# Performance work log

Measured on AMD Instinct MI355X. Metric: run time of the kernel, lower is better.

Reference implementation:

```python
import jax, jax.numpy as jnp
import numpy as np
import math

D_EMB = 1024
N_HEADS = 16
SCALE = 0.02
B, T = 4, 2048


def _norm(x):
    # torch.std_mean default: unbiased std (ddof=1) over last dim
    m = jnp.mean(x, axis=-1, keepdims=True)
    s = jnp.std(x, axis=-1, keepdims=True, ddof=1)
    return (x - m) / (s + 1e-05)


def setup_inputs() -> dict:
    key = jax.random.key(0)
    kx, kw = jax.random.split(key)
    x = jax.random.normal(kx, (B, D_EMB, T), dtype=jnp.float32)
    qkv = jax.random.normal(kw, (3, N_HEADS, D_EMB, D_EMB // N_HEADS), dtype=jnp.float32) * SCALE
    return {"x": x, "qkv": qkv}


def reference(x, qkv):
    Bsz, D, Tlen = x.shape
    H = qkv.shape[1]
    # (3, B, H, T, d_head)
    h = jnp.einsum('bdt,nhde->nbhte', x, qkv)
    q, k, v = h[0], h[1], h[2]
    q = _norm(q)
    k = _norm(k)
    scale = math.sqrt(D // H)  # torch: sqrt(d_emb // H)
    attn = jnp.einsum('bhte,bhse->bhts', q, k) / scale  # [B,H,T,T]
    attn = jax.nn.softmax(attn, axis=-1)
    out = jnp.einsum('bhts,bhse->bhet', attn, v)  # [B,H,d_head,T]
    return out.reshape(Bsz, D, Tlen)
```

## Files before the change

### kernel.cpp

```cpp
#include <hip/hip_runtime.h>
#include <hip/hip_bf16.h>

#define B_SZ 4
#define NHEADS 16
#define T_SZ 2048
#define DE 1024
#define DH 64
#define BH (B_SZ*NHEADS)
#define SCL 0.18033688011112042f

typedef __attribute__((ext_vector_type(8))) short short8;
typedef __attribute__((ext_vector_type(4))) float float4v;
typedef __attribute__((ext_vector_type(2))) unsigned int uint2v;

__device__ __forceinline__ short f2bf(float f) {
    __hip_bfloat16 h = __float2bfloat16(f);
    return *reinterpret_cast<short*>(&h);
}
__device__ __forceinline__ unsigned int pack_bf2(float a, float b) {
    float2 f; f.x = a; f.y = b;
    __hip_bfloat162 h = __float22bfloat162_rn(f);
    return *reinterpret_cast<unsigned int*>(&h);
}
__device__ __forceinline__ float4v zero4() {
    float4v z = {0.f, 0.f, 0.f, 0.f};
    return z;
}
__device__ __forceinline__ int swz(int row, int g) {
    return row * 64 + (((g) ^ (row & 7)) << 3);
}
__device__ __forceinline__ void gl_lds16(const short* g, short* l) {
    __builtin_amdgcn_global_load_lds(
        (const __attribute__((address_space(1))) void*)g,
        (__attribute__((address_space(3))) void*)l, 16, 0, 0);
}

__global__ __launch_bounds__(256) void transpose_k(const float* __restrict__ src,
                                                   short* __restrict__ dst,
                                                   int R, int C) {
    __shared__ __align__(16) short tile[64 * 65];
    int c0 = blockIdx.x * 64, r0 = blockIdx.y * 64;
    src += (size_t)blockIdx.z * R * C;
    dst += (size_t)blockIdx.z * R * C;
    int tid = threadIdx.x;
#pragma unroll
    for (int it = 0; it < 16; ++it) {
        int idx = it * 256 + tid;
        int rr = idx >> 6, cc = idx & 63;
        tile[cc * 65 + rr] = f2bf(src[(size_t)(r0 + rr) * C + c0 + cc]);
    }
    __syncthreads();
#pragma unroll
    for (int it = 0; it < 16; ++it) {
        int idx = it * 256 + tid;
        int cc = idx >> 6, rr = idx & 63;
        dst[(size_t)(c0 + cc) * R + r0 + rr] = tile[cc * 65 + rr];
    }
}

__global__ __launch_bounds__(256, 2) void qkv_k(const short* __restrict__ XT,
                                                const short* __restrict__ WT,
                                                short* __restrict__ Qw,
                                                short* __restrict__ Kw,
                                                short* __restrict__ Vt) {
    __shared__ __align__(16) short ldsA[2][128 * 64];
    __shared__ __align__(16) short ldsB[2][128 * 64];
    int b  = blockIdx.x >> 4;
    int t0 = (blockIdx.x & 15) * 128;
    int n  = blockIdx.y >> 3;
    int h0 = (blockIdx.y & 7) * 2;
    int tid = threadIdx.x, wave = tid >> 6, lane = tid & 63;
    int l15 = lane & 15, quad = lane >> 4;
    int wr = wave >> 1, wc = wave & 1;

    const short* Arow = XT + ((size_t)b * T_SZ + t0) * DE;
    const short* Brow = WT + ((size_t)n * 1024 + h0 * 64) * DE;

    int rA = lane >> 3;
    int gl = (lane & 7) ^ rA;

    float4v acc[4][4];
#pragma unroll
    for (int mm = 0; mm < 4; ++mm)
#pragma unroll
        for (int j = 0; j < 4; ++j) acc[mm][j] = zero4();

    auto STAGE = [&](short* La, short* Lb, int k0) {
#pragma unroll
        for (int it = 0; it < 4; ++it) {
            int rowbase = it * 32 + wave * 8;
            gl_lds16(&Arow[(size_t)(rowbase + rA) * DE + k0 + gl * 8],
                     &La[(it * 256 + wave * 64) * 8]);
            gl_lds16(&Brow[(size_t)(rowbase + rA) * DE + k0 + gl * 8],
                     &Lb[(it * 256 + wave * 64) * 8]);
        }
    };
    auto COMPUTE = [&](const short* La, const short* Lb) {
#pragma unroll
        for (int ks = 0; ks < 2; ++ks) {
            short8 af[4], bf[4];
#pragma unroll
            for (int mm = 0; mm < 4; ++mm)
                af[mm] = *(const short8*)&La[swz(64 * wr + 16 * mm + l15, 4 * ks + quad)];
#pragma unroll
            for (int j = 0; j < 4; ++j)
                bf[j] = *(const short8*)&Lb[swz(64 * wc + 16 * j + l15, 4 * ks + quad)];
#pragma unroll
            for (int mm = 0; mm < 4; ++mm)
#pragma unroll
                for (int j = 0; j < 4; ++j)
                    acc[mm][j] = __builtin_amdgcn_mfma_f32_16x16x32_bf16(af[mm], bf[j], acc[mm][j], 0, 0, 0);
        }
    };

    STAGE(ldsA[0], ldsB[0], 0);
    __syncthreads();
    for (int k0 = 0; k0 < DE; k0 += 128) {
        STAGE(ldsA[1], ldsB[1], k0 + 64);
        COMPUTE(ldsA[0], ldsB[0]);
        __syncthreads();
        if (k0 + 128 < DE)
            STAGE(ldsA[0], ldsB[0], k0 + 128);
        COMPUTE(ldsA[1], ldsB[1]);
        __syncthreads();
    }

    int h = h0 + wc;
    int bh = b * NHEADS + h;
#pragma unroll
    for (int mm = 0; mm < 4; ++mm) {
        int tbase = t0 + 64 * wr + 16 * mm;
        if (n < 2) {
            float oscale = (n == 0) ? SCL : 1.0f;
            float mu[4], inv[4];
#pragma unroll
            for (int r = 0; r < 4; ++r) {
                float s1 = 0.f, s2 = 0.f;
#pragma unroll
                for (int jj = 0; jj < 4; ++jj) {
                    float v = acc[mm][jj][r];
                    s1 += v; s2 += v * v;
                }
                for (int sh = 1; sh < 16; sh <<= 1) {
                    s1 += __shfl_xor(s1, sh, 64);
                    s2 += __shfl_xor(s2, sh, 64);
                }
                mu[r] = s1 * (1.0f / 64.0f);
                float var = (s2 - 64.0f * mu[r] * mu[r]) * (1.0f / 63.0f);
                var = fmaxf(var, 0.0f);
                inv[r] = oscale / (sqrtf(var) + 1e-5f);
            }
            short* dst = (n == 0 ? Qw : Kw) + (size_t)bh * T_SZ * DH;
#pragma unroll
            for (int r = 0; r < 4; ++r) {
                int t = tbase + quad * 4 + r;
#pragma unroll
                for (int jj = 0; jj < 4; ++jj) {
                    float v = (acc[mm][jj][r] - mu[r]) * inv[r];
                    dst[(size_t)t * DH + 16 * jj + l15] = f2bf(v);
                }
            }
        } else {
#pragma unroll
            for (int r = 0; r < 4; ++r) {
                int t = tbase + quad * 4 + r;
#pragma unroll
                for (int jj = 0; jj < 4; ++jj) {
                    Vt[((size_t)bh * DH + 16 * jj + l15) * T_SZ + t] =
                        f2bf(acc[mm][jj][r]);
                }
            }
        }
    }
}

__global__ __launch_bounds__(256, 4) void attn_k(const short* __restrict__ Qw,
                                                 const short* __restrict__ Kw,
                                                 const short* __restrict__ Vt,
                                                 float* __restrict__ out) {
    __shared__ __align__(16) char smem[34816];
    short* ldsK = (short*)smem;
    short* ldsV = (short*)(smem + 8192);
    short* ldsP = (short*)(smem + 16384);
    float* ldsO = (float*)smem;

    int bh = blockIdx.x;
    int t0 = blockIdx.y * 128;
    int b = bh >> 4, h = bh & 15;
    int tid = threadIdx.x, wave = tid >> 6, lane = tid & 63;
    int l15 = lane & 15, quad = lane >> 4;
    int tw = t0 + 32 * wave;

    const short* Qp = Qw + (size_t)bh * T_SZ * DH;
    const short* Kp = Kw + (size_t)bh * T_SZ * DH;
    const short* Vp = Vt + (size_t)bh * DH * T_SZ;
    short* Pw = ldsP + wave * 32 * 72;

    int rA = lane >> 3;
    int gl = (lane & 7) ^ rA;

    short8 qf[2][2];
#pragma unroll
    for (int tt = 0; tt < 2; ++tt)
#pragma unroll
        for (int ks = 0; ks < 2; ++ks)
            qf[tt][ks] = *(const short8*)&Qp[(size_t)(tw + 16 * tt + l15) * DH + ks * 32 + quad * 8];

    const short one_bf = (short)0x3F80;
    short8 ones = {one_bf, one_bf, one_bf, one_bf, one_bf, one_bf, one_bf, one_bf};

    float4v o[2][4];
    float4v ol[2];
#pragma unroll
    for (int tt = 0; tt < 2; ++tt) {
        ol[tt] = zero4();
#pragma unroll
        for (int j = 0; j < 4; ++j) o[tt][j] = zero4();
    }

    for (int s0 = 0; s0 < T_SZ; s0 += 64) {
        __syncthreads();
#pragma unroll
        for (int it = 0; it < 2; ++it) {
            int rowbase = it * 32 + wave * 8;
            gl_lds16(&Kp[(size_t)(s0 + rowbase + rA) * DH + gl * 8],
                     &ldsK[(it * 256 + wave * 64) * 8]);
            gl_lds16(&Vp[(size_t)(rowbase + rA) * T_SZ + s0 + gl * 8],
                     &ldsV[(it * 256 + wave * 64) * 8]);
        }
        __syncthreads();

#pragma unroll
        for (int j = 0; j < 4; ++j) {
            short8 k0 = *(const short8*)&ldsK[swz(16 * j + l15, quad)];
            short8 k1 = *(const short8*)&ldsK[swz(16 * j + l15, 4 + quad)];
#pragma unroll
            for (int tt = 0; tt < 2; ++tt) {
                float4v z = zero4();
                z = __builtin_amdgcn_mfma_f32_16x16x32_bf16(k0, qf[tt][0], z, 0, 0, 0);
                z = __builtin_amdgcn_mfma_f32_16x16x32_bf16(k1, qf[tt][1], z, 0, 0, 0);
                float p0 = __builtin_amdgcn_exp2f(z[0]);
                float p1 = __builtin_amdgcn_exp2f(z[1]);
                float p2 = __builtin_amdgcn_exp2f(z[2]);
                float p3 = __builtin_amdgcn_exp2f(z[3]);
                uint2v u = { pack_bf2(p0, p1), pack_bf2(p2, p3) };
                *(uint2v*)&Pw[(16 * tt + l15) * 72 + 16 * j + quad * 4] = u;
            }
        }

        short8 pf[2][2];
#pragma unroll
        for (int tt = 0; tt < 2; ++tt) {
            pf[tt][0] = *(const short8*)&Pw[(16 * tt + l15) * 72 + quad * 8];
            pf[tt][1] = *(const short8*)&Pw[(16 * tt + l15) * 72 + 32 + quad * 8];
            ol[tt] = __builtin_amdgcn_mfma_f32_16x16x32_bf16(pf[tt][0], ones, ol[tt], 0, 0, 0);
            ol[tt] = __builtin_amdgcn_mfma_f32_16x16x32_bf16(pf[tt][1], ones, ol[tt], 0, 0, 0);
        }
#pragma unroll
        for (int j = 0; j < 4; ++j) {
            short8 v0 = *(const short8*)&ldsV[swz(16 * j + l15, quad)];
            short8 v1 = *(const short8*)&ldsV[swz(16 * j + l15, 4 + quad)];
#pragma unroll
            for (int tt = 0; tt < 2; ++tt) {
                o[tt][j] = __builtin_amdgcn_mfma_f32_16x16x32_bf16(pf[tt][0], v0, o[tt][j], 0, 0, 0);
                o[tt][j] = __builtin_amdgcn_mfma_f32_16x16x32_bf16(pf[tt][1], v1, o[tt][j], 0, 0, 0);
            }
        }
    }

    float4v rinv[2];
#pragma unroll
    for (int tt = 0; tt < 2; ++tt)
#pragma unroll
        for (int r = 0; r < 4; ++r)
            rinv[tt][r] = 1.0f / ol[tt][r];

#pragma unroll
    for (int ph = 0; ph < 2; ++ph) {
        __syncthreads();
        if ((wave >> 1) == ph) {
            float* Ow = ldsO + (wave & 1) * (64 * 36);
#pragma unroll
            for (int tt = 0; tt < 2; ++tt)
#pragma unroll
                for (int j = 0; j < 4; ++j) {
                    float4v ov = o[tt][j] * rinv[tt];
                    *(float4v*)&Ow[(16 * j + l15) * 36 + 16 * tt + quad * 4] = ov;
                }
        }
        __syncthreads();
#pragma unroll
        for (int it = 0; it < 4; ++it) {
            int idx = it * 256 + tid;
            int rg = idx >> 9;
            int rid = idx & 511;
            int e = rid >> 3, t4 = (rid & 7) * 4;
            *(float4v*)&out[((size_t)(b * DE + h * DH + e)) * T_SZ + t0 + 32 * (2 * ph + rg) + t4] =
                *(const float4v*)&ldsO[rg * (64 * 36) + e * 36 + t4];
        }
    }
}

extern "C" void kernel_launch(void* const* d_in, const int* in_sizes, int n_in,
                              void* d_out, int out_size, void* d_ws, size_t ws_size,
                              hipStream_t stream) {
    const float* x = (const float*)d_in[0];
    const float* w = (const float*)d_in[1];
    float* out = (float*)d_out;
    char* ws = (char*)d_ws;

    const size_t XT_BYTES = (size_t)B_SZ * T_SZ * DE * 2;
    const size_t WT_BYTES = (size_t)3 * NHEADS * DH * DE * 2;
    const size_t QKV_BYTES = (size_t)BH * T_SZ * DH * 2;

    short* XT = (short*)(ws);
    short* WT = (short*)(ws + XT_BYTES);
    short* Qw = (short*)(ws + XT_BYTES + WT_BYTES);
    short* Kw = (short*)(ws + XT_BYTES + WT_BYTES + QKV_BYTES);
    short* Vt = (short*)(ws + XT_BYTES + WT_BYTES + 2 * QKV_BYTES);

    transpose_k<<<dim3(T_SZ / 64, DE / 64, B_SZ), 256, 0, stream>>>(x, XT, DE, T_SZ);
    transpose_k<<<dim3(1, DE / 64, 3 * NHEADS), 256, 0, stream>>>(w, WT, DE, DH);
    qkv_k<<<dim3(64, 24), 256, 0, stream>>>(XT, WT, Qw, Kw, Vt);
    attn_k<<<dim3(BH, T_SZ / 128), 256, 0, stream>>>(Qw, Kw, Vt, out);
}
```

Measured before the change: 240.3 us.

## Prefetch next K/V tile into registers during compute and pad P stride

Replaces the direct global-to-LDS K/V loads with register prefetch. The next tile is issued at the start of each iteration, then written to swizzled LDS after compute, so global latency overlaps the MFMA and exp work. It also changes the per-wave P scratch row stride from 72 to 88 to reduce LDS bank conflicts, which grows shared memory and may lower occupancy. The last iteration issues a redundant load of tile 0, and the extra register pressure could also hurt occupancy.

```diff
diff --git a/kernel.cpp b/kernel.cpp
--- a/kernel.cpp
+++ b/kernel.cpp
@@ -8,6 +8,7 @@
 #define DH 64
 #define BH (B_SZ*NHEADS)
 #define SCL 0.18033688011112042f
+#define PSTR 88
 
 typedef __attribute__((ext_vector_type(8))) short short8;
 typedef __attribute__((ext_vector_type(4))) float float4v;
@@ -178,7 +179,7 @@
                                                  const short* __restrict__ Kw,
                                                  const short* __restrict__ Vt,
                                                  float* __restrict__ out) {
-    __shared__ __align__(16) char smem[34816];
+    __shared__ __align__(16) char smem[38912];
     short* ldsK = (short*)smem;
     short* ldsV = (short*)(smem + 8192);
     short* ldsP = (short*)(smem + 16384);
@@ -194,10 +195,10 @@
     const short* Qp = Qw + (size_t)bh * T_SZ * DH;
     const short* Kp = Kw + (size_t)bh * T_SZ * DH;
     const short* Vp = Vt + (size_t)bh * DH * T_SZ;
-    short* Pw = ldsP + wave * 32 * 72;
+    short* Pw = ldsP + wave * 32 * PSTR;
 
     int rA = lane >> 3;
-    int gl = (lane & 7) ^ rA;
+    int g8 = lane & 7;
 
     short8 qf[2][2];
 #pragma unroll
@@ -218,17 +219,31 @@
         for (int j = 0; j < 4; ++j) o[tt][j] = zero4();
     }
 
-    for (int s0 = 0; s0 < T_SZ; s0 += 64) {
-        __syncthreads();
+    short8 rk[2], rv[2];
+    auto LOADNEXT = [&](int s) {
 #pragma unroll
         for (int it = 0; it < 2; ++it) {
             int rowbase = it * 32 + wave * 8;
-            gl_lds16(&Kp[(size_t)(s0 + rowbase + rA) * DH + gl * 8],
-                     &ldsK[(it * 256 + wave * 64) * 8]);
-            gl_lds16(&Vp[(size_t)(rowbase + rA) * T_SZ + s0 + gl * 8],
-                     &ldsV[(it * 256 + wave * 64) * 8]);
-        }
-        __syncthreads();
+            rk[it] = *(const short8*)&Kp[(size_t)(s + rowbase + rA) * DH + g8 * 8];
+            rv[it] = *(const short8*)&Vp[(size_t)(rowbase + rA) * T_SZ + s + g8 * 8];
+        }
+    };
+    auto WRITESTAGE = [&]() {
+#pragma unroll
+        for (int it = 0; it < 2; ++it) {
+            int rowbase = it * 32 + wave * 8;
+            *(short8*)&ldsK[swz(rowbase + rA, g8)] = rk[it];
+            *(short8*)&ldsV[swz(rowbase + rA, g8)] = rv[it];
+        }
+    };
+
+    LOADNEXT(0);
+    WRITESTAGE();
+    __syncthreads();
+
+    for (int s0 = 0; s0 < T_SZ; s0 += 64) {
+        int sn = (s0 + 64 < T_SZ) ? s0 + 64 : 0;
+        LOADNEXT(sn);
 
 #pragma unroll
         for (int j = 0; j < 4; ++j) {
@@ -244,15 +259,15 @@
                 float p2 = __builtin_amdgcn_exp2f(z[2]);
                 float p3 = __builtin_amdgcn_exp2f(z[3]);
                 uint2v u = { pack_bf2(p0, p1), pack_bf2(p2, p3) };
-                *(uint2v*)&Pw[(16 * tt + l15) * 72 + 16 * j + quad * 4] = u;
+                *(uint2v*)&Pw[(16 * tt + l15) * PSTR + 16 * j + quad * 4] = u;
             }
         }
 
         short8 pf[2][2];
 #pragma unroll
         for (int tt = 0; tt < 2; ++tt) {
-            pf[tt][0] = *(const short8*)&Pw[(16 * tt + l15) * 72 + quad * 8];
-            pf[tt][1] = *(const short8*)&Pw[(16 * tt + l15) * 72 + 32 + quad * 8];
+            pf[tt][0] = *(const short8*)&Pw[(16 * tt + l15) * PSTR + quad * 8];
+            pf[tt][1] = *(const short8*)&Pw[(16 * tt + l15) * PSTR + 32 + quad * 8];
             ol[tt] = __builtin_amdgcn_mfma_f32_16x16x32_bf16(pf[tt][0], ones, ol[tt], 0, 0, 0);
             ol[tt] = __builtin_amdgcn_mfma_f32_16x16x32_bf16(pf[tt][1], ones, ol[tt], 0, 0, 0);
         }
@@ -266,6 +281,10 @@
                 o[tt][j] = __builtin_amdgcn_mfma_f32_16x16x32_bf16(pf[tt][1], v1, o[tt][j], 0, 0, 0);
             }
         }
+
+        __syncthreads();
+        WRITESTAGE();
+        __syncthreads();
     }
 
     float4v rinv[2];
```

Result: no change. 243.7 us (+1.4%).
